# Performance work log

Measured on AMD Instinct MI355X. Metric: run time of the kernel, lower is better.

Reference implementation:

```python
import jax, jax.numpy as jnp
import numpy as np

B, E, F, Q = 8, 2000, 6000, 20
D = 256   # entity_dim == word_dim (required: word_embedding output feeds LSTM with input_size=word_dim)
WD = 256
L = 3
NUM_ENTITY, NUM_REL, NUM_WORD = 400000, 6000, 60000
NNZ = 2 * B * F
PAGERANK_LAMBDA, FACT_SCALE = 0.8, 3.0
VERY_NEG = -100000000000.0
VERY_SMALL = 1e-10


def _lin(x, W, b):
    return x @ W.T + b


def _sparse_bmm(indices, values, x, num_rows):
    # indices: [3, nnz] = (batch, row, col); x: [B, C, Dx] -> out [B, num_rows, Dx]
    b, r, c = indices[0], indices[1], indices[2]
    contrib = values[:, None] * x[b, c]
    seg = b * num_rows + r
    out = jax.ops.segment_sum(contrib, seg, num_segments=x.shape[0] * num_rows)
    return out.reshape(x.shape[0], num_rows, x.shape[2])


def _lstm(x, Wih, Whh, bih, bhh):
    # PyTorch LSTM, batch_first, 1 layer, unidirectional; gate order i,f,g,o
    Bb, T, _ = x.shape
    H = Whh.shape[1]
    def step(carry, xt):
        h, c = carry
        g = xt @ Wih.T + bih + h @ Whh.T + bhh
        i, f, gg, o = jnp.split(g, 4, axis=-1)
        c = jax.nn.sigmoid(f) * c + jax.nn.sigmoid(i) * jnp.tanh(gg)
        h = jax.nn.sigmoid(o) * jnp.tanh(c)
        return (h, c), h
    init = (jnp.zeros((Bb, H), x.dtype), jnp.zeros((Bb, H), x.dtype))
    (h, c), hs = jax.lax.scan(step, init, jnp.swapaxes(x, 0, 1))
    return jnp.swapaxes(hs, 0, 1), h


def setup_inputs():
    key = jax.random.key(0)
    ks = iter(jax.random.split(key, 48))
    p = lambda shape: jax.random.normal(next(ks), shape, jnp.float32) * 0.02
    inp = {}
    inp['local_entity'] = jax.random.randint(next(ks), (B, E), 0, NUM_ENTITY + 1)
    inp['q2e_adj_mat'] = (jax.random.uniform(next(ks), (B, E, 1)) < 0.01).astype(jnp.float32)
    inp['kb_fact_rel'] = jax.random.randint(next(ks), (B, F), 0, NUM_REL)
    inp['query_text'] = jax.random.randint(next(ks), (B, Q), 0, NUM_WORD)
    inp['answer_dist'] = (jax.random.uniform(next(ks), (B, E)) < 0.005).astype(jnp.float32)
    eb = jax.random.randint(next(ks), (NNZ,), 0, B)
    ef = jax.random.randint(next(ks), (NNZ,), 0, F)
    ee = jax.random.randint(next(ks), (NNZ,), 0, E)
    inp['e2f_indices'] = jnp.stack([eb, ef, ee])
    inp['e2f_val'] = jnp.ones((NNZ,), jnp.float32)
    fb = jax.random.randint(next(ks), (NNZ,), 0, B)
    fe = jax.random.randint(next(ks), (NNZ,), 0, E)
    ff = jax.random.randint(next(ks), (NNZ,), 0, F)
    inp['f2e_indices'] = jnp.stack([fb, fe, ff])
    inp['f2e_val'] = jnp.ones((NNZ,), jnp.float32)
    inp['entity_table'] = p((NUM_ENTITY + 1, WD)).at[-1].set(0.0)
    inp['ent_lin_W'] = p((D, WD)); inp['ent_lin_b'] = jnp.zeros((D,), jnp.float32)
    inp['relation_table'] = p((NUM_REL + 1, WD)).at[-1].set(0.0)
    inp['rel_lin_W'] = p((D, WD)); inp['rel_lin_b'] = jnp.zeros((D,), jnp.float32)
    inp['word_table'] = p((NUM_WORD + 1, D)).at[-1].set(0.0)
    inp['lstm_Wih'] = p((4 * D, WD)); inp['lstm_Whh'] = p((4 * D, D))
    inp['lstm_bih'] = jnp.zeros((4 * D,), jnp.float32); inp['lstm_bhh'] = jnp.zeros((4 * D,), jnp.float32)
    inp['q2e_W'] = p((L, D, D)); inp['q2e_b'] = jnp.zeros((L, D), jnp.float32)
    inp['e2q_W'] = p((L, D, 3 * D)); inp['e2q_b'] = jnp.zeros((L, D), jnp.float32)
    inp['e2e_W'] = p((L, D, 3 * D)); inp['e2e_b'] = jnp.zeros((L, D), jnp.float32)
    inp['head_W'] = p((L, D, D)); inp['head_b'] = jnp.zeros((L, D), jnp.float32)
    inp['tail_W'] = p((L, D, D)); inp['tail_b'] = jnp.zeros((L, D), jnp.float32)
    inp['self_W'] = p((L, D, D)); inp['self_b'] = jnp.zeros((L, D), jnp.float32)
    inp['score_W'] = p((1, D)); inp['score_b'] = jnp.zeros((1,), jnp.float32)
    return inp


def reference(local_entity, q2e_adj_mat, kb_fact_rel, query_text, answer_dist, e2f_indices, e2f_val, f2e_indices, f2e_val, entity_table, ent_lin_W, ent_lin_b, relation_table, rel_lin_W, rel_lin_b, word_table, lstm_Wih, lstm_Whh, lstm_bih, lstm_bhh, q2e_W, q2e_b, e2q_W, e2q_b, e2e_W, e2e_b, head_W, head_b, tail_W, tail_b, self_W, self_b, score_W, score_b):
    query_mask = (query_text != NUM_WORD).astype(jnp.float32)          # [B,Q]
    local_entity_mask = (local_entity != NUM_ENTITY).astype(jnp.float32)
    # query encoder (dropout = identity in eval)
    query_hidden, h_last = _lstm(word_table[query_text], lstm_Wih, lstm_Whh, lstm_bih, lstm_bhh)
    query_node_emb = h_last[:, None, :]                                # [B,1,D]
    local_fact_emb = _lin(relation_table[kb_fact_rel], rel_lin_W, rel_lin_b)  # [B,F,D]
    div = jnp.sqrt(jnp.float32(D))
    sim = jnp.einsum('bqd,bfd->bqf', query_hidden, local_fact_emb) / div
    sim = jax.nn.softmax(sim + (1.0 - query_mask)[:, :, None] * VERY_NEG, axis=1)
    att = jnp.einsum('bqf,bqd->bfd', sim, query_hidden)
    Wt = jnp.sum(att * local_fact_emb, axis=2) / div                   # [B,F]
    W_tilde = jnp.exp(Wt - jnp.max(Wt, axis=1, keepdims=True))
    e2fT = jnp.stack([e2f_indices[0], e2f_indices[2], e2f_indices[1]])  # transpose(1,2)
    e2f_softmax = _sparse_bmm(e2fT, e2f_val, W_tilde[:, :, None], E)[..., 0]
    e2f_softmax = jnp.maximum(e2f_softmax, VERY_SMALL)
    pagerank_f = q2e_adj_mat[..., 0]                                    # [B,E]
    local_entity_emb = _lin(entity_table[local_entity], ent_lin_W, ent_lin_b)  # [B,E,D]
    for i in range(L):
        q2e_emb = jnp.broadcast_to(_lin(query_node_emb, q2e_W[i], q2e_b[i]), (B, E, D))
        nxt = jnp.concatenate([local_entity_emb, q2e_emb], axis=2)
        e2f_emb = jax.nn.relu(_lin(local_fact_emb, self_W[i], self_b[i]) + _sparse_bmm(e2f_indices, e2f_val, _lin(local_entity_emb, head_W[i], head_b[i]), F))
        e2f_norm = W_tilde[:, :, None] * _sparse_bmm(e2f_indices, e2f_val, (pagerank_f / e2f_softmax)[:, :, None], F)
        e2f_emb = e2f_emb * e2f_norm
        f2e_emb = jax.nn.relu(_lin(local_entity_emb, self_W[i], self_b[i]) + _sparse_bmm(f2e_indices, f2e_val, _lin(e2f_emb, tail_W[i], tail_b[i]), E))
        pagerank_f = PAGERANK_LAMBDA * _sparse_bmm(f2e_indices, f2e_val, e2f_norm, E)[..., 0] + (1.0 - PAGERANK_LAMBDA) * pagerank_f
        nxt = jnp.concatenate([nxt, FACT_SCALE * f2e_emb], axis=2)      # [B,E,3D]
        query_node_emb = jnp.einsum('be,bed->bd', pagerank_f, _lin(nxt, e2q_W[i], e2q_b[i]))[:, None, :]
        local_entity_emb = jax.nn.relu(_lin(nxt, e2e_W[i], e2e_b[i]))
    score = _lin(local_entity_emb, score_W, score_b)[..., 0]            # [B,E]
    loss = jnp.mean(jnp.maximum(score, 0.0) - score * answer_dist + jnp.log1p(jnp.exp(-jnp.abs(score))))
    score_m = score + (1.0 - local_entity_mask) * VERY_NEG
    pred = jnp.argmax(score_m, axis=1)
    pred_dist = jax.nn.sigmoid(score_m) * local_entity_mask
    return (loss, pred, pred_dist)
```

## Files before the change

kernel.cpp:

```cpp
#include <hip/hip_runtime.h>
#include <math.h>

#define BB 8
#define EE 2000
#define FF 6000
#define QQ 20
#define DD 256
#define NENT 400000
#define NWORD 60000
#define NNZ_ 96000
#define VNEG  (-1e11f)
#define VSMALL 1e-10f

typedef __attribute__((ext_vector_type(8))) short short8v;
typedef __attribute__((ext_vector_type(4))) short short4v;
typedef __attribute__((ext_vector_type(4))) float f32x4;

__device__ __forceinline__ unsigned short f2bf_rne(float x)
{
    unsigned u = __float_as_uint(x);
    u += 0x7FFFu + ((u >> 16) & 1u);
    return (unsigned short)(u >> 16);
}
__device__ __forceinline__ float bf2f(unsigned short h)
{
    return __uint_as_float((unsigned)h << 16);
}

template<int GATHER, int DUALW, int RELU, int RS, int BIASB>
__device__ __forceinline__ void mgemm_body(
    const float* __restrict__ A1, const int* __restrict__ idx,
    const float* __restrict__ A2, float sA2,
    const short* __restrict__ W1h, const short* __restrict__ W1l,
    const short* __restrict__ W2h, const short* __restrict__ W2l,
    const float* __restrict__ biasA,
    const float* __restrict__ rowscale, const float* __restrict__ bias2,
    float* __restrict__ out, int by, int bx,
    short* __restrict__ Ah, short* __restrict__ Al)
{
    const int tid = threadIdx.x;
    const int lane = tid & 63, wv = tid >> 6;
    const int wrow = wv >> 1, wcol = wv & 1;
    const int row0 = by * 128, col0 = bx * 128;

    const int sr = tid >> 1;
    const int sko = (tid & 1) << 5;
    const int grow = row0 + sr;
    const float* aRow1 = GATHER ? A1 + (size_t)idx[grow] * 256 : A1 + (size_t)grow * 256;
    const float* aRow2 = DUALW ? A2 + (size_t)grow * 256 : nullptr;

    f32x4 acc[4][4];
    #pragma unroll
    for (int i = 0; i < 4; ++i)
        #pragma unroll
        for (int j = 0; j < 4; ++j) acc[i][j] = (f32x4){0.f, 0.f, 0.f, 0.f};

    const int nch = DUALW ? 8 : 4;
    for (int ch = 0; ch < nch; ++ch) {
        const bool hi2 = DUALW && (ch >= 4);
        const float* ar = hi2 ? aRow2 : aRow1;
        const int kbase = (ch & 3) << 6;
        #pragma unroll
        for (int q = 0; q < 8; ++q) {
            const int kc = sko + (q << 2);
            float4 a = *(const float4*)(ar + kbase + kc);
            if (DUALW && hi2) { a.x *= sA2; a.y *= sA2; a.z *= sA2; a.w *= sA2; }
            unsigned short h0 = f2bf_rne(a.x), h1 = f2bf_rne(a.y),
                           h2 = f2bf_rne(a.z), h3 = f2bf_rne(a.w);
            unsigned short l0 = f2bf_rne(a.x - bf2f(h0)), l1 = f2bf_rne(a.y - bf2f(h1)),
                           l2 = f2bf_rne(a.z - bf2f(h2)), l3 = f2bf_rne(a.w - bf2f(h3));
            const int tI = ((sr >> 4) << 1) + (kc >> 5);
            const int off = (tI << 9) + ((((sr & 15)) + (((kc >> 3) & 3) << 4)) << 3) + (kc & 7);
            *(short4v*)(Ah + off) = (short4v){(short)h0, (short)h1, (short)h2, (short)h3};
            *(short4v*)(Al + off) = (short4v){(short)l0, (short)l1, (short)l2, (short)l3};
        }
        __syncthreads();
        const short* Wh = hi2 ? W2h : W1h;
        const short* Wl = hi2 ? W2l : W1l;
        #pragma unroll
        for (int ks = 0; ks < 2; ++ks) {
            const int kg = kbase + (ks << 5) + ((lane >> 4) << 3);
            short8v bh[4], bl[4];
            #pragma unroll
            for (int ct = 0; ct < 4; ++ct) {
                const int c = col0 + (wcol << 6) + (ct << 4) + (lane & 15);
                bh[ct] = *(const short8v*)(Wh + (size_t)c * 256 + kg);
                bl[ct] = *(const short8v*)(Wl + (size_t)c * 256 + kg);
            }
            #pragma unroll
            for (int rt = 0; rt < 4; ++rt) {
                const int tI = (((wrow << 2) + rt) << 1) + ks;
                const short8v avh = *(const short8v*)(Ah + (tI << 9) + (lane << 3));
                const short8v avl = *(const short8v*)(Al + (tI << 9) + (lane << 3));
                #pragma unroll
                for (int ct = 0; ct < 4; ++ct) {
                    acc[rt][ct] = __builtin_amdgcn_mfma_f32_16x16x32_bf16(avh, bh[ct], acc[rt][ct], 0, 0, 0);
                    acc[rt][ct] = __builtin_amdgcn_mfma_f32_16x16x32_bf16(avh, bl[ct], acc[rt][ct], 0, 0, 0);
                    acc[rt][ct] = __builtin_amdgcn_mfma_f32_16x16x32_bf16(avl, bh[ct], acc[rt][ct], 0, 0, 0);
                }
            }
        }
        __syncthreads();
    }
    #pragma unroll
    for (int rt = 0; rt < 4; ++rt) {
        const int rb = row0 + (wrow << 6) + (rt << 4) + ((lane >> 4) << 2);
        #pragma unroll
        for (int ct = 0; ct < 4; ++ct) {
            const int c = col0 + (wcol << 6) + (ct << 4) + (lane & 15);
            #pragma unroll
            for (int j = 0; j < 4; ++j) {
                const int r = rb + j;
                float v = acc[rt][ct][j];
                v += BIASB ? biasA[(size_t)(r / EE) * 256 + c] : biasA[c];
                if (RS) v += rowscale[r] * bias2[c];
                if (RELU) v = fmaxf(v, 0.f);
                out[(size_t)r * 256 + c] = v;
            }
        }
    }
}

template<int GATHER, int DUALW, int RELU, int RS, int BIASB>
__global__ __launch_bounds__(256, 2) void mgemm_k(
    const float* __restrict__ A1, const int* __restrict__ idx,
    const float* __restrict__ A2, float sA2,
    const short* __restrict__ W1h, const short* __restrict__ W1l,
    const short* __restrict__ W2h, const short* __restrict__ W2l,
    const float* __restrict__ biasA,
    const float* __restrict__ rowscale, const float* __restrict__ bias2,
    float* __restrict__ out)
{
    __shared__ short Ah[16 * 512];
    __shared__ short Al[16 * 512];
    mgemm_body<GATHER, DUALW, RELU, RS, BIASB>(A1, idx, A2, sA2, W1h, W1l, W2h, W2l,
        biasA, rowscale, bias2, out, blockIdx.y, blockIdx.x, Ah, Al);
}

template<int GATHER>
__global__ __launch_bounds__(256, 2) void mgemm_pair_k(
    const float* __restrict__ Aa, const int* __restrict__ idxA,
    const short* __restrict__ Wah, const short* __restrict__ Wal,
    const float* __restrict__ ba, float* __restrict__ outa, int nya,
    const float* __restrict__ Ab, const int* __restrict__ idxB,
    const short* __restrict__ Wbh, const short* __restrict__ Wbl,
    const float* __restrict__ bb, float* __restrict__ outb)
{
    __shared__ short Ah[16 * 512];
    __shared__ short Al[16 * 512];
    const int by = blockIdx.y;
    if (by < nya)
        mgemm_body<GATHER, 0, 0, 0, 0>(Aa, idxA, nullptr, 1.f, Wah, Wal, nullptr, nullptr,
            ba, nullptr, nullptr, outa, by, blockIdx.x, Ah, Al);
    else
        mgemm_body<GATHER, 0, 0, 0, 0>(Ab, idxB, nullptr, 1.f, Wbh, Wbl, nullptr, nullptr,
            bb, nullptr, nullptr, outb, by - nya, blockIdx.x, Ah, Al);
}

__global__ void wpack_k(const float* __restrict__ relW, const float* __restrict__ entW,
                        const float* __restrict__ headW, const float* __restrict__ tailW,
                        const float* __restrict__ selfW, const float* __restrict__ e2eW,
                        short* __restrict__ wh, short* __restrict__ wl)
{
    int id = blockIdx.x * 256 + threadIdx.x;
    if (id >= 17 * 65536) return;
    int m = id >> 16, e = id & 65535;
    float x;
    if (m == 0)       x = relW[e];
    else if (m == 1)  x = entW[e];
    else if (m < 5)   x = headW[(size_t)(m - 2) * 65536 + e];
    else if (m < 8)   x = tailW[(size_t)(m - 5) * 65536 + e];
    else if (m < 11)  x = selfW[(size_t)(m - 8) * 65536 + e];
    else if (m < 14)  x = e2eW[(size_t)(m - 11) * 196608 + (size_t)(e >> 8) * 768 + (e & 255)];
    else              x = e2eW[(size_t)(m - 14) * 196608 + (size_t)(e >> 8) * 768 + 512 + (e & 255)];
    unsigned short h = f2bf_rne(x);
    wh[id] = (short)h;
    wl[id] = (short)f2bf_rne(x - bf2f(h));
}

template<int GATHER>
__global__ __launch_bounds__(256, 4) void gemm3_k(
    const float* __restrict__ A1, const int* __restrict__ idx,
    const float* __restrict__ W1, int ldw1,
    const float* __restrict__ biasA,
    float* __restrict__ out, int M, int N)
{
    __shared__ float As[16][68];
    __shared__ float Bs[16][132];
    const int tid = threadIdx.x;
    const int row0 = blockIdx.y * 64, col0 = blockIdx.x * 128;
    const int tx = tid & 15, ty = tid >> 4;
    const int srA = tid >> 2, skA = (tid & 3) << 2;
    const int srB = tid >> 1, skB = (tid & 1) << 3;
    const int grA = row0 + srA;
    const bool rvalid = (grA < M);
    const float* aRow1 = nullptr;
    if (rvalid) aRow1 = GATHER ? A1 + (size_t)idx[grA] * 256 : A1 + (size_t)grA * 256;
    const float* wR1 = W1 + (size_t)(col0 + srB) * ldw1;

    float acc[4][8];
    #pragma unroll
    for (int i = 0; i < 4; ++i)
        #pragma unroll
        for (int j = 0; j < 8; ++j) acc[i][j] = 0.f;

    float4 a0, b0, b1;
    auto fetch = [&](int ch) {
        const int k0 = ch << 4;
        if (rvalid) a0 = *(const float4*)(aRow1 + k0 + skA);
        else        a0 = make_float4(0.f, 0.f, 0.f, 0.f);
        b0 = *(const float4*)(wR1 + k0 + skB);
        b1 = *(const float4*)(wR1 + k0 + skB + 4);
    };

    fetch(0);
    for (int ch = 0; ch < 16; ++ch) {
        As[skA + 0][srA] = a0.x; As[skA + 1][srA] = a0.y;
        As[skA + 2][srA] = a0.z; As[skA + 3][srA] = a0.w;
        Bs[skB + 0][srB] = b0.x; Bs[skB + 1][srB] = b0.y;
        Bs[skB + 2][srB] = b0.z; Bs[skB + 3][srB] = b0.w;
        Bs[skB + 4][srB] = b1.x; Bs[skB + 5][srB] = b1.y;
        Bs[skB + 6][srB] = b1.z; Bs[skB + 7][srB] = b1.w;
        __syncthreads();
        if (ch + 1 < 16) fetch(ch + 1);
        #pragma unroll
        for (int kk = 0; kk < 16; ++kk) {
            float av[4], bv[8];
            *(float4*)&av[0] = *(const float4*)&As[kk][ty << 2];
            *(float4*)&bv[0] = *(const float4*)&Bs[kk][tx << 2];
            *(float4*)&bv[4] = *(const float4*)&Bs[kk][(tx << 2) + 64];
            #pragma unroll
            for (int i = 0; i < 4; ++i)
                #pragma unroll
                for (int j = 0; j < 8; ++j) acc[i][j] += av[i] * bv[j];
        }
        __syncthreads();
    }
    #pragma unroll
    for (int i = 0; i < 4; ++i) {
        int r = row0 + (ty << 2) + i;
        if (r >= M) continue;
        float* orow = out + (size_t)r * N;
        #pragma unroll
        for (int jh = 0; jh < 2; ++jh) {
            const int c = col0 + (jh << 6) + (tx << 2);
            float4 v;
            v.x = acc[i][jh * 4 + 0] + biasA[c + 0];
            v.y = acc[i][jh * 4 + 1] + biasA[c + 1];
            v.z = acc[i][jh * 4 + 2] + biasA[c + 2];
            v.w = acc[i][jh * 4 + 3] + biasA[c + 3];
            *(float4*)(orow + c) = v;
        }
    }
}

__global__ void csr_count2_k(const int* __restrict__ idxA, int* __restrict__ cntA,
                             const int* __restrict__ idxB, int* __restrict__ cntB)
{
    int k = blockIdx.x * 256 + threadIdx.x;
    if (k >= NNZ_) return;
    if (blockIdx.y == 0) atomicAdd(&cntA[idxA[k] * FF + idxA[NNZ_ + k]], 1);
    else                 atomicAdd(&cntB[idxB[k] * EE + idxB[NNZ_ + k]], 1);
}

__global__ __launch_bounds__(1024) void scan2_k(
    const int* __restrict__ cntA, int* __restrict__ rpA, int* __restrict__ curA, int nA,
    const int* __restrict__ cntB, int* __restrict__ rpB, int* __restrict__ curB, int nB)
{
    const int* cnt = blockIdx.x ? cntB : cntA;
    int* rp  = blockIdx.x ? rpB  : rpA;
    int* cur = blockIdx.x ? curB : curA;
    int n    = blockIdx.x ? nB   : nA;
    __shared__ int sums[1024];
    int t = threadIdx.x;
    int chunk = (n + 1023) / 1024;
    int lo = t * chunk, hi = lo + chunk;
    if (lo > n) lo = n;
    if (hi > n) hi = n;
    int s = 0;
    for (int i = lo; i < hi; ++i) s += cnt[i];
    sums[t] = s;
    __syncthreads();
    for (int off = 1; off < 1024; off <<= 1) {
        int v = (t >= off) ? sums[t - off] : 0;
        __syncthreads();
        sums[t] += v;
        __syncthreads();
    }
    int run = (t == 0) ? 0 : sums[t - 1];
    for (int i = lo; i < hi; ++i) { rp[i] = run; cur[i] = run; run += cnt[i]; }
    if (hi == n) rp[n] = run;
}

__global__ void csr_fill2_k(
    const int* __restrict__ idxA, const float* __restrict__ valA,
    int* __restrict__ curA, int* __restrict__ colA, float* __restrict__ vpA,
    const int* __restrict__ idxB, const float* __restrict__ valB,
    int* __restrict__ curB, int* __restrict__ colB, float* __restrict__ vpB)
{
    int k = blockIdx.x * 256 + threadIdx.x;
    if (k >= NNZ_) return;
    if (blockIdx.y == 0) {
        int row = idxA[k] * FF + idxA[NNZ_ + k];
        int p = atomicAdd(&curA[row], 1);
        colA[p] = idxA[2 * NNZ_ + k];
        vpA[p] = valA[k];
    } else {
        int row = idxB[k] * EE + idxB[NNZ_ + k];
        int p = atomicAdd(&curB[row], 1);
        colB[p] = idxB[2 * NNZ_ + k];
        vpB[p] = valB[k];
    }
}

__global__ void degw_k(const int* __restrict__ rp, const float* __restrict__ vp,
                       float* __restrict__ degw, int n)
{
    int r = blockIdx.x * 256 + threadIdx.x;
    if (r >= n) return;
    float s = 0.f;
    for (int j = rp[r]; j < rp[r + 1]; ++j) s += vp[j];
    degw[r] = s;
}

__global__ __launch_bounds__(256) void gather_fused_e2f_k(
    const int* __restrict__ rowptr, const int* __restrict__ col,
    const float* __restrict__ valp, const float* __restrict__ headsrc,
    const float* __restrict__ pr, const float* __restrict__ sm,
    const float* __restrict__ Wtil, float* __restrict__ e2fnrm,
    float* __restrict__ dst, int nrows)
{
    int gid = blockIdx.x * 256 + threadIdx.x;
    int row = gid >> 6, lane = gid & 63;
    if (row >= nrows) return;
    int b = row / FF;
    const float* prb = pr + (size_t)b * EE;
    const float* smb = sm + (size_t)b * EE;
    float4* dp = (float4*)(dst + (size_t)row * DD + (lane << 2));
    float4 acc = *dp;
    float ns = 0.f;
    int j0 = rowptr[row], j1 = rowptr[row + 1];
    for (int j = j0; j < j1; ++j) {
        int c = col[j];
        float v = valp[j];
        float4 x = *(const float4*)(headsrc + ((size_t)b * EE + c) * DD + (lane << 2));
        acc.x += v * x.x; acc.y += v * x.y; acc.z += v * x.z; acc.w += v * x.w;
        ns += v * (prb[c] / fmaxf(smb[c], VSMALL));
    }
    float nrm = Wtil[row] * ns;
    if (lane == 0) e2fnrm[row] = nrm;
    acc.x = fmaxf(acc.x, 0.f) * nrm; acc.y = fmaxf(acc.y, 0.f) * nrm;
    acc.z = fmaxf(acc.z, 0.f) * nrm; acc.w = fmaxf(acc.w, 0.f) * nrm;
    *dp = acc;
}

__global__ __launch_bounds__(256) void gather_sum_k(
    const int* __restrict__ rowptr, const int* __restrict__ col,
    const float* __restrict__ valp, const float* __restrict__ src,
    float* __restrict__ dst, int nrows, int nrPerB, int ncs)
{
    int gid = blockIdx.x * 256 + threadIdx.x;
    int row = gid >> 6, lane = gid & 63;
    if (row >= nrows) return;
    int b = row / nrPerB;
    float4 acc = make_float4(0.f, 0.f, 0.f, 0.f);
    int j0 = rowptr[row], j1 = rowptr[row + 1];
    for (int j = j0; j < j1; ++j) {
        int c = col[j];
        float v = valp[j];
        float4 x = *(const float4*)(src + ((size_t)b * ncs + c) * DD + (lane << 2));
        acc.x += v * x.x; acc.y += v * x.y; acc.z += v * x.z; acc.w += v * x.w;
    }
    *(float4*)(dst + (size_t)row * DD + (lane << 2)) = acc;
}

__global__ void transpose_whh_k(const float* __restrict__ Whh, float* __restrict__ WhhT)
{
    int i = blockIdx.x * 256 + threadIdx.x;
    int k = i >> 10, j = i & 1023;
    WhhT[i] = Whh[(size_t)j * 256 + k];
}

__global__ __launch_bounds__(256) void lstm_k(
    const float* __restrict__ Xg, const float* __restrict__ WhhT,
    const float* __restrict__ bhh, float* __restrict__ qh, float* __restrict__ qne)
{
    __shared__ float h[DD];
    __shared__ float gs[4 * DD];
    const int b = blockIdx.x, t = threadIdx.x;
    h[t] = 0.f;
    float c = 0.f;
    const float4 bb4 = *(const float4*)(bhh + 4 * t);
    const float4* wt4 = (const float4*)WhhT + t;
    __syncthreads();
    for (int step = 0; step < QQ; ++step) {
        float a0 = 0.f, a1 = 0.f, a2 = 0.f, a3 = 0.f;
        #pragma unroll 16
        for (int k = 0; k < DD; ++k) {
            float4 w = wt4[k * 256];
            float hk = h[k];
            a0 += w.x * hk; a1 += w.y * hk; a2 += w.z * hk; a3 += w.w * hk;
        }
        float4 xg = *(const float4*)(Xg + ((size_t)b * QQ + step) * 1024 + 4 * t);
        float4 g4 = make_float4(a0 + xg.x + bb4.x, a1 + xg.y + bb4.y,
                                a2 + xg.z + bb4.z, a3 + xg.w + bb4.w);
        *(float4*)(gs + 4 * t) = g4;
        __syncthreads();
        float gi = gs[t], gf = gs[DD + t], gg = gs[2 * DD + t], go = gs[3 * DD + t];
        float si = 1.f / (1.f + expf(-gi));
        float sf = 1.f / (1.f + expf(-gf));
        float so = 1.f / (1.f + expf(-go));
        c = sf * c + si * tanhf(gg);
        float hh = so * tanhf(c);
        h[t] = hh;
        qh[((size_t)b * QQ + step) * DD + t] = hh;
        __syncthreads();
    }
    qne[(size_t)b * DD + t] = h[t];
}

__global__ __launch_bounds__(256) void simwt_k(
    const float* __restrict__ qhid, const int* __restrict__ qtext,
    const float* __restrict__ lfe, float* __restrict__ Wt)
{
    __shared__ float qs[QQ * DD];
    __shared__ float qmn[QQ];
    const int b = blockIdx.y;
    const int f = blockIdx.x * 256 + threadIdx.x;
    for (int i = threadIdx.x; i < QQ * DD; i += 256) qs[i] = qhid[(size_t)b * QQ * DD + i];
    if (threadIdx.x < QQ)
        qmn[threadIdx.x] = (qtext[b * QQ + threadIdx.x] != NWORD) ? 0.f : VNEG;
    __syncthreads();
    if (f >= FF) return;
    float acc[QQ];
    #pragma unroll
    for (int q = 0; q < QQ; ++q) acc[q] = 0.f;
    const float* lr = lfe + ((size_t)b * FF + f) * DD;
    for (int d = 0; d < DD; d += 4) {
        float4 x = *(const float4*)(lr + d);
        #pragma unroll
        for (int q = 0; q < QQ; ++q) {
            float4 y = *(const float4*)&qs[q * DD + d];
            acc[q] += x.x * y.x + x.y * y.y + x.z * y.z + x.w * y.w;
        }
    }
    const float inv = 0.0625f;
    float pre[QQ], m = -INFINITY;
    #pragma unroll
    for (int q = 0; q < QQ; ++q) { pre[q] = acc[q] * inv + qmn[q]; m = fmaxf(m, pre[q]); }
    float s = 0.f;
    #pragma unroll
    for (int q = 0; q < QQ; ++q) s += expf(pre[q] - m);
    float wt = 0.f;
    #pragma unroll
    for (int q = 0; q < QQ; ++q) wt += (expf(pre[q] - m) / s) * (acc[q] * inv);
    Wt[(size_t)b * FF + f] = wt;
}

__global__ __launch_bounds__(256) void rowmax_wtil_k(
    const float* __restrict__ Wt, float* __restrict__ Wtil)
{
    __shared__ float red[256];
    int b = blockIdx.x, t = threadIdx.x;
    float m = -INFINITY;
    for (int f = t; f < FF; f += 256) m = fmaxf(m, Wt[b * FF + f]);
    red[t] = m; __syncthreads();
    for (int s = 128; s > 0; s >>= 1) {
        if (t < s) red[t] = fmaxf(red[t], red[t + s]);
        __syncthreads();
    }
    float mx = red[0];
    for (int f = t; f < FF; f += 256) Wtil[b * FF + f] = expf(Wt[b * FF + f] - mx);
}

__global__ void scatter_sm_k(const int* __restrict__ idx, const float* __restrict__ val,
                             const float* __restrict__ Wtil, float* __restrict__ dst)
{
    int k = blockIdx.x * 256 + threadIdx.x;
    if (k >= NNZ_) return;
    int b = idx[k], e = idx[2 * NNZ_ + k], f = idx[NNZ_ + k];
    atomicAdd(&dst[(size_t)b * EE + e], val[k] * Wtil[(size_t)b * FF + f]);
}

__global__ __launch_bounds__(256) void qlin_ebias_k(
    const float* __restrict__ qne, const float* __restrict__ q2eW,
    const float* __restrict__ q2eb, const float* __restrict__ e2eW,
    const float* __restrict__ e2eb, float* __restrict__ qlin, float* __restrict__ ebias)
{
    __shared__ float xs[DD], qs[DD];
    int b = blockIdx.x, j = threadIdx.x;
    xs[j] = qne[b * DD + j];
    __syncthreads();
    float acc = q2eb[j];
    const float* wr = q2eW + (size_t)j * DD;
    #pragma unroll 4
    for (int k = 0; k < DD; ++k) acc += xs[k] * wr[k];
    qlin[b * DD + j] = acc;
    qs[j] = acc;
    __syncthreads();
    float acc2 = e2eb[j];
    const float* wr2 = e2eW + (size_t)j * 768 + 256;
    #pragma unroll 4
    for (int k = 0; k < DD; ++k) acc2 += qs[k] * wr2[k];
    ebias[b * DD + j] = acc2;
}

#define VCH 80
#define NCHK (EE / VCH)
__global__ __launch_bounds__(256) void vreduce_pr_k(
    const int* __restrict__ f2e_rp, const int* __restrict__ f2e_col,
    const float* __restrict__ f2e_vp, const float* __restrict__ e2fnrm,
    float* __restrict__ pr, const float* __restrict__ lee,
    const float* __restrict__ f2e, float* __restrict__ vpartL,
    float* __restrict__ vpartF, float* __restrict__ vpartS)
{
    int b = blockIdx.y, ch = blockIdx.x, k = threadIdx.x;
    int e0 = ch * VCH;
    __shared__ float prs[VCH];
    if (k < VCH) {
        int row = b * EE + e0 + k;
        float s = 0.f;
        for (int j = f2e_rp[row]; j < f2e_rp[row + 1]; ++j)
            s += f2e_vp[j] * e2fnrm[(size_t)b * FF + f2e_col[j]];
        float v = 0.8f * s + 0.2f * pr[row];
        pr[row] = v;
        prs[k] = v;
    }
    __syncthreads();
    float a1 = 0.f, a2 = 0.f;
    for (int e = 0; e < VCH; ++e) {
        float p = prs[e];
        size_t base = ((size_t)b * EE + e0 + e) * DD + k;
        a1 += p * lee[base];
        a2 += p * f2e[base];
    }
    int pi = ch * BB + b;
    vpartL[(size_t)pi * DD + k] = a1;
    vpartF[(size_t)pi * DD + k] = a2;
    float sp = 0.f;
    for (int e = k; e < VCH; e += 256) sp += prs[e];
    __shared__ float red[256];
    red[k] = sp; __syncthreads();
    for (int s = 128; s > 0; s >>= 1) {
        if (k < s) red[k] += red[k + s];
        __syncthreads();
    }
    if (k == 0) vpartS[pi] = red[0];
}

__global__ __launch_bounds__(256) void qneupd_qlin_k(
    const float* __restrict__ vpartL, const float* __restrict__ vpartF,
    const float* __restrict__ vpartS, const float* __restrict__ qlinCur,
    const float* __restrict__ W, const float* __restrict__ bias,
    float* __restrict__ qne,
    const float* __restrict__ q2eWn, const float* __restrict__ q2ebn,
    const float* __restrict__ e2eWn, const float* __restrict__ e2ebn,
    float* __restrict__ qlinNext, float* __restrict__ ebiasNext, int hasNext)
{
    __shared__ float s1[DD], s2[DD], s3[DD], qn[DD], qs[DD];
    int b = blockIdx.x, j = threadIdx.x;
    float a1 = 0.f, a3 = 0.f, sp = 0.f;
    for (int ch = 0; ch < NCHK; ++ch) {
        int pi = ch * BB + b;
        a1 += vpartL[(size_t)pi * DD + j];
        a3 += vpartF[(size_t)pi * DD + j];
        sp += vpartS[pi];
    }
    s1[j] = a1; s2[j] = qlinCur[b * DD + j]; s3[j] = a3;
    __syncthreads();
    float acc = sp * bias[j];
    const float* wr = W + (size_t)j * 768;
    #pragma unroll 4
    for (int k = 0; k < DD; ++k)
        acc += s1[k] * wr[k] + sp * s2[k] * wr[256 + k] + 3.f * s3[k] * wr[512 + k];
    qne[b * DD + j] = acc;
    if (!hasNext) return;
    qn[j] = acc;
    __syncthreads();
    float aq = q2ebn[j];
    const float* wq = q2eWn + (size_t)j * DD;
    #pragma unroll 4
    for (int k = 0; k < DD; ++k) aq += qn[k] * wq[k];
    qlinNext[b * DD + j] = aq;
    qs[j] = aq;
    __syncthreads();
    float ae = e2ebn[j];
    const float* we = e2eWn + (size_t)j * 768 + 256;
    #pragma unroll 4
    for (int k = 0; k < DD; ++k) ae += qs[k] * we[k];
    ebiasNext[b * DD + j] = ae;
}

__global__ __launch_bounds__(256) void final2_k(
    const float* __restrict__ lee, const float* __restrict__ sw_,
    const float* __restrict__ sb, const int* __restrict__ local_entity,
    const float* __restrict__ ans, float* __restrict__ out, float* __restrict__ losspart)
{
    __shared__ float sw[DD];
    int b = blockIdx.x, t = threadIdx.x;
    sw[t] = sw_[t];
    __syncthreads();
    float sb0 = sb[0];
    float lsum = 0.f, bm = -INFINITY;
    int bi = EE;
    for (int e = t; e < EE; e += 256) {
        const float* a = lee + ((size_t)b * EE + e) * DD;
        float s = sb0;
        for (int k = 0; k < DD; k += 4) {
            float4 v = *(const float4*)(a + k);
            s += v.x * sw[k] + v.y * sw[k + 1] + v.z * sw[k + 2] + v.w * sw[k + 3];
        }
        float mask = (local_entity[b * EE + e] != NENT) ? 1.f : 0.f;
        float smv = s + (1.f - mask) * VNEG;
        float sig;
        if (smv >= 0.f) sig = 1.f / (1.f + expf(-smv));
        else { float es = expf(smv); sig = es / (1.f + es); }
        out[1 + BB + b * EE + e] = sig * mask;
        lsum += fmaxf(s, 0.f) - s * ans[b * EE + e] + log1pf(expf(-fabsf(s)));
        if (smv > bm) { bm = smv; bi = e; }
    }
    __shared__ float rv[256]; __shared__ int ri[256]; __shared__ float rl[256];
    rv[t] = bm; ri[t] = bi; rl[t] = lsum;
    __syncthreads();
    for (int s = 128; s > 0; s >>= 1) {
        if (t < s) {
            rl[t] += rl[t + s];
            if (rv[t + s] > rv[t] || (rv[t + s] == rv[t] && ri[t + s] < ri[t])) {
                rv[t] = rv[t + s]; ri[t] = ri[t + s];
            }
        }
        __syncthreads();
    }
    if (t == 0) { losspart[b] = rl[0]; out[1 + b] = (float)ri[0]; }
}

__global__ void loss_k(const float* __restrict__ losspart, float* __restrict__ out)
{
    if (threadIdx.x == 0) {
        float s = 0.f;
        for (int b = 0; b < BB; ++b) s += losspart[b];
        out[0] = s / (float)(BB * EE);
    }
}

extern "C" void kernel_launch(void* const* d_in, const int* in_sizes, int n_in,
                              void* d_out, int out_size, void* d_ws, size_t ws_size,
                              hipStream_t stream)
{
    (void)in_sizes; (void)n_in; (void)out_size; (void)ws_size;
    const int*   local_entity = (const int*)d_in[0];
    const float* q2e_adj      = (const float*)d_in[1];
    const int*   kb_fact_rel  = (const int*)d_in[2];
    const int*   query_text   = (const int*)d_in[3];
    const float* answer_dist  = (const float*)d_in[4];
    const int*   e2f_idx      = (const int*)d_in[5];
    const float* e2f_val      = (const float*)d_in[6];
    const int*   f2e_idx      = (const int*)d_in[7];
    const float* f2e_val      = (const float*)d_in[8];
    const float* entity_table = (const float*)d_in[9];
    const float* ent_W        = (const float*)d_in[10];
    const float* ent_b        = (const float*)d_in[11];
    const float* rel_table    = (const float*)d_in[12];
    const float* rel_W        = (const float*)d_in[13];
    const float* rel_b        = (const float*)d_in[14];
    const float* word_table   = (const float*)d_in[15];
    const float* Wih          = (const float*)d_in[16];
    const float* Whh          = (const float*)d_in[17];
    const float* bih          = (const float*)d_in[18];
    const float* bhh          = (const float*)d_in[19];
    const float* q2e_W        = (const float*)d_in[20];
    const float* q2e_b        = (const float*)d_in[21];
    const float* e2q_W        = (const float*)d_in[22];
    const float* e2q_b        = (const float*)d_in[23];
    const float* e2e_W        = (const float*)d_in[24];
    const float* e2e_b        = (const float*)d_in[25];
    const float* head_W       = (const float*)d_in[26];
    const float* head_b       = (const float*)d_in[27];
    const float* tail_W       = (const float*)d_in[28];
    const float* tail_b       = (const float*)d_in[29];
    const float* self_W       = (const float*)d_in[30];
    const float* self_b       = (const float*)d_in[31];
    const float* score_W      = (const float*)d_in[32];
    const float* score_b      = (const float*)d_in[33];

    const int NR1 = BB * FF;
    const int NR2 = BB * EE;

    float* ws = (float*)d_ws;
    size_t off = 0;
    auto alloc = [&](size_t n) { float* p = ws + off; off += n; return p; };
    auto salloc = [&](size_t nshorts) { short* p = (short*)(ws + off); off += nshorts / 2; return p; };
    float* Xg      = alloc((size_t)BB * QQ * 1024);
    float* WhhT    = alloc((size_t)1024 * DD);
    float* qh      = alloc((size_t)BB * QQ * DD);
    float* qne     = alloc(BB * DD);
    float* lfe     = alloc((size_t)NR1 * DD);
    float* leeA    = alloc((size_t)NR2 * DD);
    float* leeB    = alloc((size_t)NR2 * DD);
    float* Wt      = alloc(BB * FF);
    float* Wtil    = alloc(BB * FF);
    float* e2fsm   = alloc(BB * EE);
    float* pr      = alloc(BB * EE);
    float* qlinA   = alloc(BB * DD);
    float* qlinB   = alloc(BB * DD);
    float* ebiasA  = alloc(BB * DD);
    float* ebiasB  = alloc(BB * DD);
    float* e2fnrm  = alloc(BB * FF);
    float* losspart= alloc(8);
    float* bufC    = alloc((size_t)NR2 * DD);
    float* e2fT    = alloc((size_t)NR1 * DD);
    float* f2eT    = alloc((size_t)NR2 * DD);
    float* tmp     = alloc((size_t)NR2 * DD);
    float* vpartL  = alloc((size_t)NCHK * BB * DD);
    float* vpartF  = alloc((size_t)NCHK * BB * DD);
    float* vpartS  = alloc(NCHK * BB);
    float* degw2   = alloc(NR2);
    float* e2f_vp  = alloc(NNZ_);
    float* f2e_vp  = alloc(NNZ_);
    short* wbh     = salloc((size_t)17 * 65536);
    short* wbl     = salloc((size_t)17 * 65536);
    int* ib = (int*)(ws + off);
    size_t ioff = 0;
    auto ialloc = [&](size_t n) { int* p = ib + ioff; ioff += n; return p; };
    int* e2f_cnt = ialloc(NR1);
    int* e2f_rp  = ialloc(NR1 + 1);
    int* e2f_cur = ialloc(NR1);
    int* e2f_col = ialloc(NNZ_);
    int* f2e_cnt = ialloc(NR2);
    int* f2e_rp  = ialloc(NR2 + 1);
    int* f2e_cur = ialloc(NR2);
    int* f2e_col = ialloc(NNZ_);

    auto WH = [&](int m) { return wbh + (size_t)m * 65536; };
    auto WL = [&](int m) { return wbl + (size_t)m * 65536; };

    float* outp = (float*)d_out;
    const int SCB = (NNZ_ + 255) / 256;

    wpack_k<<<(17 * 65536) / 256, 256, 0, stream>>>(rel_W, ent_W, head_W, tail_W,
                                                    self_W, e2e_W, wbh, wbl);

    hipMemsetAsync(e2f_cnt, 0, NR1 * sizeof(int), stream);
    hipMemsetAsync(f2e_cnt, 0, NR2 * sizeof(int), stream);
    csr_count2_k<<<dim3(SCB, 2), 256, 0, stream>>>(e2f_idx, e2f_cnt, f2e_idx, f2e_cnt);
    scan2_k<<<2, 1024, 0, stream>>>(e2f_cnt, e2f_rp, e2f_cur, NR1,
                                    f2e_cnt, f2e_rp, f2e_cur, NR2);
    csr_fill2_k<<<dim3(SCB, 2), 256, 0, stream>>>(
        e2f_idx, e2f_val, e2f_cur, e2f_col, e2f_vp,
        f2e_idx, f2e_val, f2e_cur, f2e_col, f2e_vp);
    degw_k<<<(NR2 + 255) / 256, 256, 0, stream>>>(f2e_rp, f2e_vp, degw2, NR2);

    gemm3_k<1><<<dim3(8, 3), 256, 0, stream>>>(
        word_table, query_text, Wih, 256, bih, Xg, BB * QQ, 1024);
    transpose_whh_k<<<1024, 256, 0, stream>>>(Whh, WhhT);
    lstm_k<<<BB, 256, 0, stream>>>(Xg, WhhT, bhh, qh, qne);

    mgemm_pair_k<1><<<dim3(2, 375 + 125), 256, 0, stream>>>(
        rel_table, kb_fact_rel, WH(0), WL(0), rel_b, lfe, 375,
        entity_table, local_entity, WH(1), WL(1), ent_b, leeA);

    simwt_k<<<dim3((FF + 255) / 256, BB), 256, 0, stream>>>(qh, query_text, lfe, Wt);
    rowmax_wtil_k<<<BB, 256, 0, stream>>>(Wt, Wtil);

    hipMemsetAsync(e2fsm, 0, BB * EE * sizeof(float), stream);
    scatter_sm_k<<<SCB, 256, 0, stream>>>(e2f_idx, e2f_val, Wtil, e2fsm);

    hipMemcpyAsync(pr, q2e_adj, BB * EE * sizeof(float), hipMemcpyDeviceToDevice, stream);
    qlin_ebias_k<<<BB, 256, 0, stream>>>(qne, q2e_W, q2e_b, e2e_W, e2e_b, qlinA, ebiasA);

    float* lee = leeA;   float* lee2 = leeB;
    float* qlinCur = qlinA;  float* qlinNxt = qlinB;
    float* ebiasCur = ebiasA; float* ebiasNxt = ebiasB;

    for (int i = 0; i < 3; ++i) {
        const float* e2qWi  = e2q_W  + (size_t)i * DD * 3 * DD;
        const float* e2qbi  = e2q_b  + i * DD;
        const float* headbi = head_b + i * DD;
        const float* tailbi = tail_b + i * DD;
        const float* selfbi = self_b + i * DD;

        mgemm_pair_k<0><<<dim3(2, 125 + 375), 256, 0, stream>>>(
            lee, nullptr, WH(2 + i), WL(2 + i), headbi, bufC, 125,
            lfe, nullptr, WH(8 + i), WL(8 + i), selfbi, e2fT);

        gather_fused_e2f_k<<<(NR1 * 64) / 256, 256, 0, stream>>>(
            e2f_rp, e2f_col, e2f_vp, bufC, pr, e2fsm, Wtil, e2fnrm, e2fT, NR1);

        gather_sum_k<<<(NR2 * 64) / 256, 256, 0, stream>>>(
            f2e_rp, f2e_col, f2e_vp, e2fT, tmp, NR2, EE, FF);

        mgemm_k<0, 1, 1, 1, 0><<<dim3(2, 125), 256, 0, stream>>>(
            lee, nullptr, tmp, 1.f, WH(8 + i), WL(8 + i), WH(5 + i), WL(5 + i),
            selfbi, degw2, tailbi, f2eT);

        vreduce_pr_k<<<dim3(NCHK, BB), 256, 0, stream>>>(
            f2e_rp, f2e_col, f2e_vp, e2fnrm, pr, lee, f2eT, vpartL, vpartF, vpartS);

        int hasNext = (i < 2) ? 1 : 0;
        const float* q2eWn = q2e_W + (size_t)(i + 1) * DD * DD * (hasNext ? 1 : 0);
        const float* q2ebn = q2e_b + (i + 1) * DD * (hasNext ? 1 : 0);
        const float* e2eWn = e2e_W + (size_t)(i + 1) * DD * 3 * DD * (hasNext ? 1 : 0);
        const float* e2ebn = e2e_b + (i + 1) * DD * (hasNext ? 1 : 0);
        qneupd_qlin_k<<<BB, 256, 0, stream>>>(
            vpartL, vpartF, vpartS, qlinCur, e2qWi, e2qbi, qne,
            q2eWn, q2ebn, e2eWn, e2ebn, qlinNxt, ebiasNxt, hasNext);

        mgemm_k<0, 1, 1, 0, 1><<<dim3(2, 125), 256, 0, stream>>>(
            lee, nullptr, f2eT, 3.f, WH(11 + i), WL(11 + i), WH(14 + i), WL(14 + i),
            ebiasCur, nullptr, nullptr, lee2);
        { float* t = lee; lee = lee2; lee2 = t; }
        { float* t = qlinCur; qlinCur = qlinNxt; qlinNxt = t; }
        { float* t = ebiasCur; ebiasCur = ebiasNxt; ebiasNxt = t; }
    }

    final2_k<<<BB, 256, 0, stream>>>(lee, score_W, score_b, local_entity,
                                     answer_dist, outp, losspart);
    loss_k<<<1, 64, 0, stream>>>(losspart, outp);
}
```

Baseline: 1.295 ms.

## Split LSTM recurrence across 64 blocks with LDS-resident weights and grid barrier

Each batch item's recurrent matvec is distributed over 8 blocks. Each block caches a 128-row slice of Whh in shared memory instead of rereading the full matrix from global memory every step. Gate pre-activations are exchanged through a double-buffered global buffer with a spin-wait atomic grid barrier each timestep. This removes the separate transpose kernel and the serial bandwidth cost. It relies on all 64 blocks being co-resident and adds barrier latency per step.

```diff
diff --git a/kernel.cpp b/kernel.cpp
--- a/kernel.cpp
+++ b/kernel.cpp
@@ -374,49 +374,77 @@
     *(float4*)(dst + (size_t)row * DD + (lane << 2)) = acc;
 }
 
-__global__ void transpose_whh_k(const float* __restrict__ Whh, float* __restrict__ WhhT)
-{
-    int i = blockIdx.x * 256 + threadIdx.x;
-    int k = i >> 10, j = i & 1023;
-    WhhT[i] = Whh[(size_t)j * 256 + k];
-}
-
-__global__ __launch_bounds__(256) void lstm_k(
-    const float* __restrict__ Xg, const float* __restrict__ WhhT,
-    const float* __restrict__ bhh, float* __restrict__ qh, float* __restrict__ qne)
-{
-    __shared__ float h[DD];
-    __shared__ float gs[4 * DD];
-    const int b = blockIdx.x, t = threadIdx.x;
-    h[t] = 0.f;
-    float c = 0.f;
-    const float4 bb4 = *(const float4*)(bhh + 4 * t);
-    const float4* wt4 = (const float4*)WhhT + t;
-    __syncthreads();
+#define LSTM_BLOCKS 64
+__global__ __launch_bounds__(256, 1) void lstm2_k(
+    const float* __restrict__ Xg, const float* __restrict__ Whh,
+    const float* __restrict__ bhh, float* __restrict__ gbuf,
+    unsigned* __restrict__ bar, float* __restrict__ qh, float* __restrict__ qne)
+{
+    __shared__ float wslice[128 * 257];
+    __shared__ float hbuf[256];
+    __shared__ float cbuf[256];
+    __shared__ float gpart[256];
+    const int B = blockIdx.x;
+    const int b = B >> 3, p = B & 7;
+    const int t = threadIdx.x;
+    const float* wsrc = Whh + (size_t)p * 128 * 256;
+    for (int i = t; i < 128 * 64; i += 256) {
+        int row = i >> 6, q4 = (i & 63) << 2;
+        float4 w = *(const float4*)(wsrc + (size_t)row * 256 + q4);
+        float* d = &wslice[row * 257 + q4];
+        d[0] = w.x; d[1] = w.y; d[2] = w.z; d[3] = w.w;
+    }
+    hbuf[t] = 0.f; cbuf[t] = 0.f;
+    __syncthreads();
+
+    unsigned* bar_cnt = bar;
+    unsigned* bar_gen = bar + 1;
+
     for (int step = 0; step < QQ; ++step) {
-        float a0 = 0.f, a1 = 0.f, a2 = 0.f, a3 = 0.f;
-        #pragma unroll 16
-        for (int k = 0; k < DD; ++k) {
-            float4 w = wt4[k * 256];
-            float hk = h[k];
-            a0 += w.x * hk; a1 += w.y * hk; a2 += w.z * hk; a3 += w.w * hk;
-        }
-        float4 xg = *(const float4*)(Xg + ((size_t)b * QQ + step) * 1024 + 4 * t);
-        float4 g4 = make_float4(a0 + xg.x + bb4.x, a1 + xg.y + bb4.y,
-                                a2 + xg.z + bb4.z, a3 + xg.w + bb4.w);
-        *(float4*)(gs + 4 * t) = g4;
-        __syncthreads();
-        float gi = gs[t], gf = gs[DD + t], gg = gs[2 * DD + t], go = gs[3 * DD + t];
-        float si = 1.f / (1.f + expf(-gi));
-        float sf = 1.f / (1.f + expf(-gf));
-        float so = 1.f / (1.f + expf(-go));
-        c = sf * c + si * tanhf(gg);
-        float hh = so * tanhf(c);
-        h[t] = hh;
-        qh[((size_t)b * QQ + step) * DD + t] = hh;
-        __syncthreads();
-    }
-    qne[(size_t)b * DD + t] = h[t];
+        {
+            const int r = t & 127, half = t >> 7;
+            const float* wr = &wslice[r * 257 + half * 128];
+            const float* hb = &hbuf[half * 128];
+            float acc = 0.f;
+            #pragma unroll 8
+            for (int k = 0; k < 128; ++k) acc += wr[k] * hb[k];
+            gpart[t] = acc;
+        }
+        __syncthreads();
+        if (t < 128) {
+            const int gr = p * 128 + t;
+            float g = bhh[gr] + Xg[((size_t)b * QQ + step) * 1024 + gr]
+                    + gpart[t] + gpart[t + 128];
+            gbuf[((size_t)(step & 1) * BB + b) * 1024 + gr] = g;
+        }
+        __syncthreads();
+        if (t == 0) {
+            __threadfence();
+            const unsigned target = (unsigned)(step + 1) * LSTM_BLOCKS;
+            unsigned old = atomicAdd(bar_cnt, 1u);
+            if (old == target - 1u) {
+                atomicExch(bar_gen, (unsigned)(step + 1));
+            } else {
+                while (atomicAdd(bar_gen, 0u) < (unsigned)(step + 1)) {}
+            }
+            __threadfence();
+        }
+        __syncthreads();
+        {
+            const float* g = gbuf + ((size_t)(step & 1) * BB + b) * 1024;
+            float gi = g[t], gf = g[256 + t], gg = g[512 + t], go = g[768 + t];
+            float si = 1.f / (1.f + expf(-gi));
+            float sf = 1.f / (1.f + expf(-gf));
+            float so = 1.f / (1.f + expf(-go));
+            float c = sf * cbuf[t] + si * tanhf(gg);
+            float hh = so * tanhf(c);
+            cbuf[t] = c;
+            hbuf[t] = hh;
+            if (p == 0) qh[((size_t)b * QQ + step) * DD + t] = hh;
+        }
+        __syncthreads();
+    }
+    if (p == 0) qne[(size_t)b * DD + t] = hbuf[t];
 }
 
 __global__ __launch_bounds__(256) void simwt_k(
@@ -689,9 +717,9 @@
     float* ws = (float*)d_ws;
     size_t off = 0;
     auto alloc = [&](size_t n) { float* p = ws + off; off += n; return p; };
-    auto salloc = [&](size_t nshorts) { short* p = (short*)(ws + off); off += nshorts / 2; return p; };
+    auto salloc = [&](size_t nshorts) { short* p = (short*)(ws + off); off += (nshorts + 1) / 2; return p; };
     float* Xg      = alloc((size_t)BB * QQ * 1024);
-    float* WhhT    = alloc((size_t)1024 * DD);
+    float* gbuf    = alloc((size_t)2 * BB * 1024);
     float* qh      = alloc((size_t)BB * QQ * DD);
     float* qne     = alloc(BB * DD);
     float* lfe     = alloc((size_t)NR1 * DD);
@@ -730,6 +758,7 @@
     int* f2e_rp  = ialloc(NR2 + 1);
     int* f2e_cur = ialloc(NR2);
     int* f2e_col = ialloc(NNZ_);
+    unsigned* bar = (unsigned*)ialloc(2);
 
     auto WH = [&](int m) { return wbh + (size_t)m * 65536; };
     auto WL = [&](int m) { return wbl + (size_t)m * 65536; };
@@ -752,8 +781,8 @@
 
     gemm3_k<1><<<dim3(8, 3), 256, 0, stream>>>(
         word_table, query_text, Wih, 256, bih, Xg, BB * QQ, 1024);
-    transpose_whh_k<<<1024, 256, 0, stream>>>(Whh, WhhT);
-    lstm_k<<<BB, 256, 0, stream>>>(Xg, WhhT, bhh, qh, qne);
+    hipMemsetAsync(bar, 0, 2 * sizeof(unsigned), stream);
+    lstm2_k<<<LSTM_BLOCKS, 256, 0, stream>>>(Xg, Whh, bhh, gbuf, bar, qh, qne);
 
     mgemm_pair_k<1><<<dim3(2, 375 + 125), 256, 0, stream>>>(
         rel_table, kb_fact_rel, WH(0), WL(0), rel_b, lfe, 375,
```

New measurement: 1.259 ms. -2.8%, faster.
